# Kernel optimization log

Measured on AMD Instinct MI355X. Metric: run time of the kernel, lower is better.

The kernel has to match this reference:

```python
import jax, jax.numpy as jnp
import numpy as np

HIDDEN = 1024
HEADS = 16
HEAD_DIM = HIDDEN // HEADS


def setup_inputs() -> dict:
    key = jax.random.key(0)
    ks = jax.random.split(key, 9)
    B, S = 2, 2048
    std = 0.02
    inp = {
        "query": jax.random.normal(ks[0], (B, S, HIDDEN), dtype=jnp.float32),
        "Wq": jax.random.normal(ks[1], (HIDDEN, HIDDEN), dtype=jnp.float32) * std,
        "bq": jnp.zeros((HIDDEN,), dtype=jnp.float32),
        "Wk": jax.random.normal(ks[2], (HIDDEN, HIDDEN), dtype=jnp.float32) * std,
        "bk": jnp.zeros((HIDDEN,), dtype=jnp.float32),
        "Wv": jax.random.normal(ks[3], (HIDDEN, HIDDEN), dtype=jnp.float32) * std,
        "bv": jnp.zeros((HIDDEN,), dtype=jnp.float32),
        "Wo": jax.random.normal(ks[4], (HIDDEN, HIDDEN), dtype=jnp.float32) * std,
        "bo": jnp.zeros((HIDDEN,), dtype=jnp.float32),
    }
    return inp


def reference(query, Wq, bq, Wk, bk, Wv, bv, Wo, bo):
    B, S, H = query.shape
    # torch nn.Linear: y = x @ W.T + b
    Q = query @ Wq.T + bq
    K = query @ Wk.T + bk  # key defaults to query (self-attention)
    V = query @ Wv.T + bv
    # [B, S, H] -> [B, heads, S, head_dim]
    def split_heads(x):
        return x.reshape(B, S, HEADS, HEAD_DIM).transpose(0, 2, 1, 3)
    Qh, Kh, Vh = split_heads(Q), split_heads(K), split_heads(V)
    scale = jnp.sqrt(jnp.asarray(HEAD_DIM, dtype=query.dtype))
    scores = jnp.einsum("bhqd,bhkd->bhqk", Qh, Kh) / scale
    attn = jax.nn.softmax(scores, axis=-1)  # dropout=0 (eval)
    context = jnp.einsum("bhqk,bhkd->bhqd", attn, Vh)
    context = context.transpose(0, 2, 1, 3).reshape(B, S, H)
    output = context @ Wo.T + bo
    return output, attn
```

## Files before the change

### kernel.cpp

```cpp
#include <hip/hip_runtime.h>
#include <hip/hip_bf16.h>
#include <cstdint>

typedef __attribute__((ext_vector_type(4))) float f32x4;
typedef __attribute__((ext_vector_type(8))) short bf16x8;

__device__ __forceinline__ unsigned short f2bf(float f){
  union { float f; unsigned int u; } v; v.f = f;
  unsigned int u = v.u;
  u += 0x7FFFu + ((u >> 16) & 1u);
  return (unsigned short)(u >> 16);
}
__device__ __forceinline__ float bf2f(unsigned short s){
  union { unsigned int u; float f; } v; v.u = ((unsigned int)s) << 16;
  return v.f;
}

__global__ __launch_bounds__(256) void cvt_bf16(const float* __restrict__ in,
                                                unsigned short* __restrict__ out,
                                                int n4){
  int i = blockIdx.x * 256 + threadIdx.x;
  if (i < n4){
    float4 v = ((const float4*)in)[i];
    ushort4 o;
    o.x = f2bf(v.x); o.y = f2bf(v.y); o.z = f2bf(v.z); o.w = f2bf(v.w);
    ((ushort4*)out)[i] = o;
  }
}

__global__ __launch_bounds__(256) void qkv_gemm(
    const unsigned short* __restrict__ A,
    const unsigned short* __restrict__ W0,
    const unsigned short* __restrict__ W1,
    const unsigned short* __restrict__ W2,
    const float* __restrict__ b0,
    const float* __restrict__ b1,
    const float* __restrict__ b2,
    unsigned short* __restrict__ Qo,
    unsigned short* __restrict__ Khead,
    unsigned short* __restrict__ Vto)
{
  __shared__ unsigned short As[2][128*64];
  __shared__ unsigned short Bs[2][128*64];

  const int K = 1024;
  const int tid = threadIdx.x;
  const int l   = tid & 63;
  const int wid = tid >> 6;
  const int g   = l >> 4;
  const int li  = l & 15;
  const int widx = blockIdx.x >> 3;
  const int m0  = blockIdx.y * 128;
  const int n0  = (blockIdx.x & 7) * 128;
  const int wm  = (wid >> 1) * 64;
  const int wn  = (wid & 1) * 64;
  const int srow = tid >> 3;
  const int sck  = tid & 7;

  const unsigned short* Bw = (widx == 0) ? W0 : ((widx == 1) ? W1 : W2);
  const float* bias        = (widx == 0) ? b0 : ((widx == 1) ? b1 : b2);

  const unsigned short* Ag = A  + (size_t)(m0 + srow) * K + sck * 8;
  const unsigned short* Bg = Bw + (size_t)(n0 + srow) * K + sck * 8;

  f32x4 acc[4][4] = {};
  bf16x8 ra[4], rb[4];
  const int NT = K >> 6;

  #pragma unroll
  for (int r = 0; r < 4; ++r){
    ra[r] = *(const bf16x8*)(Ag + (size_t)(r*32) * K);
    rb[r] = *(const bf16x8*)(Bg + (size_t)(r*32) * K);
  }
  #pragma unroll
  for (int r = 0; r < 4; ++r){
    const int row = srow + r*32;
    const int ck  = sck ^ (row & 7);
    *(bf16x8*)(&As[0][row*64 + ck*8]) = ra[r];
    *(bf16x8*)(&Bs[0][row*64 + ck*8]) = rb[r];
  }
  __syncthreads();

  int cur = 0;
  for (int kt = 0; kt < NT; ++kt){
    if (kt + 1 < NT){
      const int kof = (kt + 1) << 6;
      #pragma unroll
      for (int r = 0; r < 4; ++r){
        ra[r] = *(const bf16x8*)(Ag + (size_t)(r*32) * K + kof);
        rb[r] = *(const bf16x8*)(Bg + (size_t)(r*32) * K + kof);
      }
    }
    #pragma unroll
    for (int kk = 0; kk < 2; ++kk){
      bf16x8 af[4], bfr[4];
      #pragma unroll
      for (int f = 0; f < 4; ++f){
        const int rowa = wm + f*16 + li;
        const int cka  = (kk*4 + g) ^ (rowa & 7);
        af[f] = *(const bf16x8*)(&As[cur][rowa*64 + cka*8]);
        const int rowb = wn + f*16 + li;
        const int ckb  = (kk*4 + g) ^ (rowb & 7);
        bfr[f] = *(const bf16x8*)(&Bs[cur][rowb*64 + ckb*8]);
      }
      #pragma unroll
      for (int fm = 0; fm < 4; ++fm)
        #pragma unroll
        for (int fn = 0; fn < 4; ++fn)
          acc[fm][fn] = __builtin_amdgcn_mfma_f32_16x16x32_bf16(af[fm], bfr[fn], acc[fm][fn], 0, 0, 0);
    }
    __syncthreads();
    if (kt + 1 < NT){
      #pragma unroll
      for (int r = 0; r < 4; ++r){
        const int row = srow + r*32;
        const int ck  = sck ^ (row & 7);
        *(bf16x8*)(&As[cur^1][row*64 + ck*8]) = ra[r];
        *(bf16x8*)(&Bs[cur^1][row*64 + ck*8]) = rb[r];
      }
      __syncthreads();
    }
    cur ^= 1;
  }

  #pragma unroll
  for (int fn = 0; fn < 4; ++fn){
    const int col = n0 + wn + fn*16 + li;
    const float bv = bias[col];
    #pragma unroll
    for (int fm = 0; fm < 4; ++fm){
      #pragma unroll
      for (int j = 0; j < 4; ++j){
        const int row = m0 + wm + fm*16 + g*4 + j;
        const float v = acc[fm][fn][j] + bv;
        const int bb = row >> 11;
        const int s  = row & 2047;
        if (widx == 0){
          Qo[(size_t)row * 1024 + col] = f2bf(v);
        } else if (widx == 1){
          const int hh = col >> 6, dd = col & 63;
          Khead[(((size_t)(bb*16 + hh))*2048 + s)*64 + dd] = f2bf(v);
        } else {
          Vto[((size_t)(bb*1024 + col)) * 2048 + s] = f2bf(v);
        }
      }
    }
  }
}

__global__ __launch_bounds__(256) void gemm_bt(
    const unsigned short* __restrict__ A,
    const unsigned short* __restrict__ Bw,
    const float* __restrict__ bias,
    float* __restrict__ outp,
    int M, int N, int K)
{
  __shared__ unsigned short As[2][128*64];
  __shared__ unsigned short Bs[2][128*64];

  const int tid = threadIdx.x;
  const int l   = tid & 63;
  const int wid = tid >> 6;
  const int g   = l >> 4;
  const int li  = l & 15;
  const int m0  = blockIdx.y * 128;
  const int n0  = blockIdx.x * 128;
  const int wm  = (wid >> 1) * 64;
  const int wn  = (wid & 1) * 64;
  const int srow = tid >> 3;
  const int sck  = tid & 7;

  const unsigned short* Ag = A  + (size_t)(m0 + srow) * K + sck * 8;
  const unsigned short* Bg = Bw + (size_t)(n0 + srow) * K + sck * 8;

  f32x4 acc[4][4] = {};
  bf16x8 ra[4], rb[4];
  const int NT = K >> 6;

  #pragma unroll
  for (int r = 0; r < 4; ++r){
    ra[r] = *(const bf16x8*)(Ag + (size_t)(r*32) * K);
    rb[r] = *(const bf16x8*)(Bg + (size_t)(r*32) * K);
  }
  #pragma unroll
  for (int r = 0; r < 4; ++r){
    const int row = srow + r*32;
    const int ck  = sck ^ (row & 7);
    *(bf16x8*)(&As[0][row*64 + ck*8]) = ra[r];
    *(bf16x8*)(&Bs[0][row*64 + ck*8]) = rb[r];
  }
  __syncthreads();

  int cur = 0;
  for (int kt = 0; kt < NT; ++kt){
    if (kt + 1 < NT){
      const int kof = (kt + 1) << 6;
      #pragma unroll
      for (int r = 0; r < 4; ++r){
        ra[r] = *(const bf16x8*)(Ag + (size_t)(r*32) * K + kof);
        rb[r] = *(const bf16x8*)(Bg + (size_t)(r*32) * K + kof);
      }
    }
    #pragma unroll
    for (int kk = 0; kk < 2; ++kk){
      bf16x8 af[4], bfr[4];
      #pragma unroll
      for (int f = 0; f < 4; ++f){
        const int rowa = wm + f*16 + li;
        const int cka  = (kk*4 + g) ^ (rowa & 7);
        af[f] = *(const bf16x8*)(&As[cur][rowa*64 + cka*8]);
        const int rowb = wn + f*16 + li;
        const int ckb  = (kk*4 + g) ^ (rowb & 7);
        bfr[f] = *(const bf16x8*)(&Bs[cur][rowb*64 + ckb*8]);
      }
      #pragma unroll
      for (int fm = 0; fm < 4; ++fm)
        #pragma unroll
        for (int fn = 0; fn < 4; ++fn)
          acc[fm][fn] = __builtin_amdgcn_mfma_f32_16x16x32_bf16(af[fm], bfr[fn], acc[fm][fn], 0, 0, 0);
    }
    __syncthreads();
    if (kt + 1 < NT){
      #pragma unroll
      for (int r = 0; r < 4; ++r){
        const int row = srow + r*32;
        const int ck  = sck ^ (row & 7);
        *(bf16x8*)(&As[cur^1][row*64 + ck*8]) = ra[r];
        *(bf16x8*)(&Bs[cur^1][row*64 + ck*8]) = rb[r];
      }
      __syncthreads();
    }
    cur ^= 1;
  }

  #pragma unroll
  for (int fn = 0; fn < 4; ++fn){
    const int col = n0 + wn + fn*16 + li;
    const float bv = bias[col];
    #pragma unroll
    for (int fm = 0; fm < 4; ++fm){
      #pragma unroll
      for (int j = 0; j < 4; ++j){
        const int row = m0 + wm + fm*16 + g*4 + j;
        outp[(size_t)row * N + col] = acc[fm][fn][j] + bv;
      }
    }
  }
}

__global__ __launch_bounds__(256, 4) void attn_denom(
    const unsigned short* __restrict__ Qb,
    const unsigned short* __restrict__ Khead,
    float* __restrict__ denomP)
{
  __shared__ unsigned short Ks[256*64];
  char* Kb8 = (char*)Ks;

  const int tid = threadIdx.x;
  const int l   = tid & 63;
  const int w   = tid >> 6;
  const int g   = l >> 4;
  const int li  = l & 15;
  const int kt  = blockIdx.x >> 5;
  const int bh  = blockIdx.x & 31;
  const int qt  = blockIdx.y;
  const int b   = bh >> 4;
  const int h   = bh & 15;

  {
    const unsigned short* Kg = Khead + ((size_t)bh * 2048 + kt*256) * 64;
    #pragma unroll
    for (int p = 0; p < 8; ++p){
      const int key = p*32 + (tid >> 3);
      const int c   = tid & 7;
      const bf16x8 v = *(const bf16x8*)(Kg + (size_t)key * 64 + c*8);
      *(bf16x8*)(Kb8 + key*128 + ((c ^ (key & 7)) * 16)) = v;
    }
  }
  __syncthreads();

  #pragma unroll
  for (int rg = 0; rg < 2; ++rg){
    const int qrow = qt*128 + w*32 + rg*16 + li;
    const size_t qoff = (size_t)(b*2048 + qrow) * 1024 + h*64 + g*8;
    const bf16x8 aq0 = *(const bf16x8*)(Qb + qoff);
    const bf16x8 aq1 = *(const bf16x8*)(Qb + qoff + 32);

    float ls = 0.f;
    #pragma unroll
    for (int cf = 0; cf < 16; ++cf){
      const int key = cf*16 + li;
      const bf16x8 k0 = *(const bf16x8*)(Kb8 + key*128 + (( g    ^ (key & 7)) * 16));
      const bf16x8 k1 = *(const bf16x8*)(Kb8 + key*128 + (((g+4) ^ (key & 7)) * 16));
      f32x4 t = {};
      t = __builtin_amdgcn_mfma_f32_16x16x32_bf16(k0, aq0, t, 0, 0, 0);
      t = __builtin_amdgcn_mfma_f32_16x16x32_bf16(k1, aq1, t, 0, 0, 0);
      ls += __expf(t[0]*0.125f) + __expf(t[1]*0.125f)
          + __expf(t[2]*0.125f) + __expf(t[3]*0.125f);
    }
    ls += __shfl_xor(ls, 16);
    ls += __shfl_xor(ls, 32);
    if (l < 16)
      denomP[((size_t)kt*32 + bh)*2048 + qt*128 + w*32 + rg*16 + l] = ls;
  }
}

__global__ __launch_bounds__(256, 2) void attn_pass(
    const unsigned short* __restrict__ Qb,
    const unsigned short* __restrict__ Khead,
    const unsigned short* __restrict__ Vt,
    const float* __restrict__ denomP,
    float* __restrict__ attn,
    float* __restrict__ CP)
{
  __shared__ unsigned short Ks[256*64];
  __shared__ __align__(16) unsigned short Pw4[4][16*256];
  char* Kb8 = (char*)Ks;

  const int tid = threadIdx.x;
  const int l   = tid & 63;
  const int w   = tid >> 6;
  const int g   = l >> 4;
  const int li  = l & 15;
  const int kt  = blockIdx.x >> 5;
  const int bh  = blockIdx.x & 31;
  const int qt  = blockIdx.y;
  const int b   = bh >> 4;
  const int h   = bh & 15;

  {
    const unsigned short* Kg = Khead + ((size_t)bh * 2048 + kt*256) * 64;
    #pragma unroll
    for (int p = 0; p < 8; ++p){
      const int key = p*32 + (tid >> 3);
      const int c   = tid & 7;
      const bf16x8 v = *(const bf16x8*)(Kg + (size_t)key * 64 + c*8);
      *(bf16x8*)(Kb8 + key*128 + ((c ^ (key & 7)) * 16)) = v;
    }
  }
  __syncthreads();

  char* myP = (char*)(&Pw4[w][0]);
  const int swz = (li & 7) << 3;
  const unsigned short* Vbase = Vt + (size_t)(b*1024 + h*64) * 2048 + kt*256;

  f32x4 acc0[4] = {};
  f32x4 acc1[4] = {};

  #pragma unroll
  for (int rg = 0; rg < 2; ++rg){
    const int qbase = qt*128 + w*32 + rg*16;
    const int qrow  = qbase + li;

    float ds = 0.f;
    #pragma unroll
    for (int k2 = 0; k2 < 8; ++k2)
      ds += denomP[((size_t)k2*32 + bh)*2048 + qrow];
    const float rv = 1.0f / ds;

    const size_t qoff = (size_t)(b*2048 + qrow) * 1024 + h*64 + g*8;
    const bf16x8 aq0 = *(const bf16x8*)(Qb + qoff);
    const bf16x8 aq1 = *(const bf16x8*)(Qb + qoff + 32);

    #pragma unroll
    for (int cf = 0; cf < 16; ++cf){
      const int key = cf*16 + li;
      const bf16x8 k0 = *(const bf16x8*)(Kb8 + key*128 + (( g    ^ (key & 7)) * 16));
      const bf16x8 k1 = *(const bf16x8*)(Kb8 + key*128 + (((g+4) ^ (key & 7)) * 16));
      f32x4 t = {};
      t = __builtin_amdgcn_mfma_f32_16x16x32_bf16(k0, aq0, t, 0, 0, 0);
      t = __builtin_amdgcn_mfma_f32_16x16x32_bf16(k1, aq1, t, 0, 0, 0);
      ushort4 u;
      u.x = f2bf(__expf(t[0]*0.125f) * rv);
      u.y = f2bf(__expf(t[1]*0.125f) * rv);
      u.z = f2bf(__expf(t[2]*0.125f) * rv);
      u.w = f2bf(__expf(t[3]*0.125f) * rv);
      const int colb = cf*32 + g*8;
      *(ushort4*)(myP + li*512 + (colb ^ swz)) = u;
    }

    #pragma unroll
    for (int r = 0; r < 16; ++r){
      const ushort4 u = *(const ushort4*)(myP + r*512 + ((l*8) ^ ((r & 7) << 3)));
      f32x4 o;
      o[0] = bf2f(u.x); o[1] = bf2f(u.y); o[2] = bf2f(u.z); o[3] = bf2f(u.w);
      *(f32x4*)(attn + ((size_t)bh*2048 + qbase + r)*2048 + kt*256 + l*4) = o;
    }

    #pragma unroll
    for (int ks = 0; ks < 8; ++ks){
      const int colb2 = ks*64 + g*16;
      const ushort4 plo = *(const ushort4*)(myP + li*512 + ( colb2      ^ swz));
      const ushort4 phi = *(const ushort4*)(myP + li*512 + ((colb2 + 8) ^ swz));
      bf16x8 pa;
      pa[0] = plo.x; pa[1] = plo.y; pa[2] = plo.z; pa[3] = plo.w;
      pa[4] = phi.x; pa[5] = phi.y; pa[6] = phi.z; pa[7] = phi.w;
      #pragma unroll
      for (int df = 0; df < 4; ++df){
        const bf16x8 vb = *(const bf16x8*)(Vbase + (size_t)(df*16 + li) * 2048 + ks*32 + g*8);
        if (rg == 0) acc0[df] = __builtin_amdgcn_mfma_f32_16x16x32_bf16(vb, pa, acc0[df], 0, 0, 0);
        else         acc1[df] = __builtin_amdgcn_mfma_f32_16x16x32_bf16(vb, pa, acc1[df], 0, 0, 0);
      }
    }
  }

  #pragma unroll
  for (int rg = 0; rg < 2; ++rg){
    const int qrow = qt*128 + w*32 + rg*16 + li;
    #pragma unroll
    for (int df = 0; df < 4; ++df){
      const f32x4 v = (rg == 0) ? acc0[df] : acc1[df];
      *(f32x4*)(CP + (((size_t)kt*32 + bh)*2048 + qrow)*64 + df*16 + g*4) = v;
    }
  }
}

__global__ __launch_bounds__(256) void ctx_reduce(
    const float* __restrict__ CP,
    unsigned short* __restrict__ Cb)
{
  const int idx = blockIdx.x * 256 + threadIdx.x;
  const int bh  = idx >> 15;
  const int rem = idx & 32767;
  const int q   = rem >> 4;
  const int d4  = (rem & 15) << 2;
  f32x4 s = {};
  #pragma unroll
  for (int kt = 0; kt < 8; ++kt){
    const f32x4 v = *(const f32x4*)(CP + (((size_t)kt*32 + bh)*2048 + q)*64 + d4);
    s[0] += v[0]; s[1] += v[1]; s[2] += v[2]; s[3] += v[3];
  }
  const int b = bh >> 4, h = bh & 15;
  ushort4 o;
  o.x = f2bf(s[0]); o.y = f2bf(s[1]); o.z = f2bf(s[2]); o.w = f2bf(s[3]);
  *(ushort4*)(Cb + (size_t)(b*2048 + q)*1024 + h*64 + d4) = o;
}

extern "C" void kernel_launch(void* const* d_in, const int* in_sizes, int n_in,
                              void* d_out, int out_size, void* d_ws, size_t ws_size,
                              hipStream_t stream)
{
  const float* X  = (const float*)d_in[0];
  const float* Wq = (const float*)d_in[1];
  const float* bq = (const float*)d_in[2];
  const float* Wk = (const float*)d_in[3];
  const float* bk = (const float*)d_in[4];
  const float* Wv = (const float*)d_in[5];
  const float* bv = (const float*)d_in[6];
  const float* Wo = (const float*)d_in[7];
  const float* bo = (const float*)d_in[8];

  char* ws = (char*)d_ws;
  unsigned short* Xb    = (unsigned short*)(ws);
  unsigned short* Qb    = (unsigned short*)(ws + (size_t)( 8u<<20));
  unsigned short* Khead = (unsigned short*)(ws + (size_t)(16u<<20));
  unsigned short* Vt    = (unsigned short*)(ws + (size_t)(24u<<20));
  unsigned short* Cb    = (unsigned short*)(ws + (size_t)(32u<<20));
  unsigned short* Wqb   = (unsigned short*)(ws + (size_t)(40u<<20));
  unsigned short* Wkb   = (unsigned short*)(ws + (size_t)(42u<<20));
  unsigned short* Wvb   = (unsigned short*)(ws + (size_t)(44u<<20));
  unsigned short* Wob   = (unsigned short*)(ws + (size_t)(46u<<20));
  float*          denomP= (float*)(ws + (size_t)(48u<<20));
  float*          CP    = (float*)(ws + (size_t)(56u<<20));

  float* out  = (float*)d_out;
  float* attn = out + (size_t)4194304;

  cvt_bf16<<<4096, 256, 0, stream>>>(X,  Xb,  1048576);
  cvt_bf16<<<1024, 256, 0, stream>>>(Wq, Wqb, 262144);
  cvt_bf16<<<1024, 256, 0, stream>>>(Wk, Wkb, 262144);
  cvt_bf16<<<1024, 256, 0, stream>>>(Wv, Wvb, 262144);
  cvt_bf16<<<1024, 256, 0, stream>>>(Wo, Wob, 262144);

  dim3 qkvgrid(24, 32);
  qkv_gemm<<<qkvgrid, 256, 0, stream>>>(Xb, Wqb, Wkb, Wvb, bq, bk, bv, Qb, Khead, Vt);

  dim3 agrid(256, 16);
  attn_denom<<<agrid, 256, 0, stream>>>(Qb, Khead, denomP);
  attn_pass<<<agrid, 256, 0, stream>>>(Qb, Khead, Vt, denomP, attn, CP);

  ctx_reduce<<<4096, 256, 0, stream>>>(CP, Cb);

  dim3 ggrid(8, 32);
  gemm_bt<<<ggrid, 256, 0, stream>>>(Cb, Wob, bo, out, 4096, 1024, 1024);
}
```

Measured before the change: 363.5 us.

## Fuse attention denominator, probability pass and context reduction into one kernel

Replaces the separate denominator kernel, the split-key attention pass and the context reduction kernel with a single kernel. Each block owns 64 query rows of one head and loops over all eight key tiles twice: once for the softmax denominator, once to write probabilities and accumulate P·V in registers. This removes the partial-denominator and partial-context buffers, their global round trips and two launches. In exchange there are fewer blocks (1024 vs 4096), serialized key-tile loops with barriers, and the K tiles are reloaded for the second pass. It also pads the K rows in shared memory, batches the V loads, and uses nontemporal stores for the attention output.

```diff
diff --git a/kernel.cpp b/kernel.cpp
--- a/kernel.cpp
+++ b/kernel.cpp
@@ -248,125 +248,87 @@
   }
 }
 
-__global__ __launch_bounds__(256, 4) void attn_denom(
+__global__ __launch_bounds__(256, 2) void attn_all(
     const unsigned short* __restrict__ Qb,
     const unsigned short* __restrict__ Khead,
-    float* __restrict__ denomP)
+    const unsigned short* __restrict__ Vt,
+    float* __restrict__ attn,
+    unsigned short* __restrict__ ctxb)
 {
-  __shared__ unsigned short Ks[256*64];
-  char* Kb8 = (char*)Ks;
+  __shared__ __align__(16) char Kb8[256*144];
+  __shared__ __align__(16) unsigned short Pw4[4][16*256];
 
   const int tid = threadIdx.x;
   const int l   = tid & 63;
   const int w   = tid >> 6;
   const int g   = l >> 4;
   const int li  = l & 15;
-  const int kt  = blockIdx.x >> 5;
   const int bh  = blockIdx.x & 31;
-  const int qt  = blockIdx.y;
+  const int qt  = blockIdx.x >> 5;
   const int b   = bh >> 4;
   const int h   = bh & 15;
 
-  {
-    const unsigned short* Kg = Khead + ((size_t)bh * 2048 + kt*256) * 64;
-    #pragma unroll
-    for (int p = 0; p < 8; ++p){
-      const int key = p*32 + (tid >> 3);
-      const int c   = tid & 7;
-      const bf16x8 v = *(const bf16x8*)(Kg + (size_t)key * 64 + c*8);
-      *(bf16x8*)(Kb8 + key*128 + ((c ^ (key & 7)) * 16)) = v;
-    }
-  }
-  __syncthreads();
-
-  #pragma unroll
-  for (int rg = 0; rg < 2; ++rg){
-    const int qrow = qt*128 + w*32 + rg*16 + li;
-    const size_t qoff = (size_t)(b*2048 + qrow) * 1024 + h*64 + g*8;
-    const bf16x8 aq0 = *(const bf16x8*)(Qb + qoff);
-    const bf16x8 aq1 = *(const bf16x8*)(Qb + qoff + 32);
-
-    float ls = 0.f;
+  const int qrow = qt*64 + w*16 + li;
+  const size_t qoff = (size_t)(b*2048 + qrow) * 1024 + h*64 + g*8;
+  const bf16x8 aq0 = *(const bf16x8*)(Qb + qoff);
+  const bf16x8 aq1 = *(const bf16x8*)(Qb + qoff + 32);
+  const unsigned short* Kg0 = Khead + (size_t)bh * (2048*64);
+
+  float ls = 0.f;
+  for (int kt = 0; kt < 8; ++kt){
+    __syncthreads();
+    {
+      const unsigned short* Kg = Kg0 + (size_t)kt * (256*64);
+      #pragma unroll
+      for (int p = 0; p < 8; ++p){
+        const int key = p*32 + (tid >> 3);
+        const int c   = tid & 7;
+        const bf16x8 v = *(const bf16x8*)(Kg + (size_t)key*64 + c*8);
+        *(bf16x8*)(Kb8 + key*144 + ((c ^ (key & 7)) * 16)) = v;
+      }
+    }
+    __syncthreads();
     #pragma unroll
     for (int cf = 0; cf < 16; ++cf){
       const int key = cf*16 + li;
-      const bf16x8 k0 = *(const bf16x8*)(Kb8 + key*128 + (( g    ^ (key & 7)) * 16));
-      const bf16x8 k1 = *(const bf16x8*)(Kb8 + key*128 + (((g+4) ^ (key & 7)) * 16));
+      const bf16x8 k0 = *(const bf16x8*)(Kb8 + key*144 + (( g    ^ (key & 7)) * 16));
+      const bf16x8 k1 = *(const bf16x8*)(Kb8 + key*144 + (((g+4) ^ (key & 7)) * 16));
       f32x4 t = {};
       t = __builtin_amdgcn_mfma_f32_16x16x32_bf16(k0, aq0, t, 0, 0, 0);
       t = __builtin_amdgcn_mfma_f32_16x16x32_bf16(k1, aq1, t, 0, 0, 0);
       ls += __expf(t[0]*0.125f) + __expf(t[1]*0.125f)
           + __expf(t[2]*0.125f) + __expf(t[3]*0.125f);
     }
-    ls += __shfl_xor(ls, 16);
-    ls += __shfl_xor(ls, 32);
-    if (l < 16)
-      denomP[((size_t)kt*32 + bh)*2048 + qt*128 + w*32 + rg*16 + l] = ls;
-  }
-}
-
-__global__ __launch_bounds__(256, 2) void attn_pass(
-    const unsigned short* __restrict__ Qb,
-    const unsigned short* __restrict__ Khead,
-    const unsigned short* __restrict__ Vt,
-    const float* __restrict__ denomP,
-    float* __restrict__ attn,
-    float* __restrict__ CP)
-{
-  __shared__ unsigned short Ks[256*64];
-  __shared__ __align__(16) unsigned short Pw4[4][16*256];
-  char* Kb8 = (char*)Ks;
-
-  const int tid = threadIdx.x;
-  const int l   = tid & 63;
-  const int w   = tid >> 6;
-  const int g   = l >> 4;
-  const int li  = l & 15;
-  const int kt  = blockIdx.x >> 5;
-  const int bh  = blockIdx.x & 31;
-  const int qt  = blockIdx.y;
-  const int b   = bh >> 4;
-  const int h   = bh & 15;
-
-  {
-    const unsigned short* Kg = Khead + ((size_t)bh * 2048 + kt*256) * 64;
-    #pragma unroll
-    for (int p = 0; p < 8; ++p){
-      const int key = p*32 + (tid >> 3);
-      const int c   = tid & 7;
-      const bf16x8 v = *(const bf16x8*)(Kg + (size_t)key * 64 + c*8);
-      *(bf16x8*)(Kb8 + key*128 + ((c ^ (key & 7)) * 16)) = v;
-    }
-  }
-  __syncthreads();
-
+  }
+  ls += __shfl_xor(ls, 16);
+  ls += __shfl_xor(ls, 32);
+  const float rv = 1.0f / ls;
+
+  f32x4 pv[4] = {};
   char* myP = (char*)(&Pw4[w][0]);
   const int swz = (li & 7) << 3;
-  const unsigned short* Vbase = Vt + (size_t)(b*1024 + h*64) * 2048 + kt*256;
-
-  f32x4 acc0[4] = {};
-  f32x4 acc1[4] = {};
-
-  #pragma unroll
-  for (int rg = 0; rg < 2; ++rg){
-    const int qbase = qt*128 + w*32 + rg*16;
-    const int qrow  = qbase + li;
-
-    float ds = 0.f;
-    #pragma unroll
-    for (int k2 = 0; k2 < 8; ++k2)
-      ds += denomP[((size_t)k2*32 + bh)*2048 + qrow];
-    const float rv = 1.0f / ds;
-
-    const size_t qoff = (size_t)(b*2048 + qrow) * 1024 + h*64 + g*8;
-    const bf16x8 aq0 = *(const bf16x8*)(Qb + qoff);
-    const bf16x8 aq1 = *(const bf16x8*)(Qb + qoff + 32);
+  const unsigned short* Vb0 = Vt + (size_t)(b*1024 + h*64) * 2048;
+  float* arow0 = attn + ((size_t)bh*2048 + qt*64 + w*16) * 2048;
+
+  for (int kt = 0; kt < 8; ++kt){
+    __syncthreads();
+    {
+      const unsigned short* Kg = Kg0 + (size_t)kt * (256*64);
+      #pragma unroll
+      for (int p = 0; p < 8; ++p){
+        const int key = p*32 + (tid >> 3);
+        const int c   = tid & 7;
+        const bf16x8 v = *(const bf16x8*)(Kg + (size_t)key*64 + c*8);
+        *(bf16x8*)(Kb8 + key*144 + ((c ^ (key & 7)) * 16)) = v;
+      }
+    }
+    __syncthreads();
 
     #pragma unroll
     for (int cf = 0; cf < 16; ++cf){
       const int key = cf*16 + li;
-      const bf16x8 k0 = *(const bf16x8*)(Kb8 + key*128 + (( g    ^ (key & 7)) * 16));
-      const bf16x8 k1 = *(const bf16x8*)(Kb8 + key*128 + (((g+4) ^ (key & 7)) * 16));
+      const bf16x8 k0 = *(const bf16x8*)(Kb8 + key*144 + (( g    ^ (key & 7)) * 16));
+      const bf16x8 k1 = *(const bf16x8*)(Kb8 + key*144 + (((g+4) ^ (key & 7)) * 16));
       f32x4 t = {};
       t = __builtin_amdgcn_mfma_f32_16x16x32_bf16(k0, aq0, t, 0, 0, 0);
       t = __builtin_amdgcn_mfma_f32_16x16x32_bf16(k1, aq1, t, 0, 0, 0);
@@ -375,8 +337,30 @@
       u.y = f2bf(__expf(t[1]*0.125f) * rv);
       u.z = f2bf(__expf(t[2]*0.125f) * rv);
       u.w = f2bf(__expf(t[3]*0.125f) * rv);
-      const int colb = cf*32 + g*8;
-      *(ushort4*)(myP + li*512 + (colb ^ swz)) = u;
+      *(ushort4*)(myP + li*512 + ((cf*32 + g*8) ^ swz)) = u;
+    }
+
+    #pragma unroll
+    for (int vh = 0; vh < 2; ++vh){
+      bf16x8 vb[16];
+      #pragma unroll
+      for (int ks = 0; ks < 4; ++ks)
+        #pragma unroll
+        for (int df = 0; df < 4; ++df)
+          vb[ks*4+df] = *(const bf16x8*)(Vb0 + (size_t)(df*16 + li)*2048
+                                         + kt*256 + (vh*4+ks)*32 + g*8);
+      #pragma unroll
+      for (int ks = 0; ks < 4; ++ks){
+        const int colb = (vh*4+ks)*64 + g*16;
+        const ushort4 plo = *(const ushort4*)(myP + li*512 + ( colb      ^ swz));
+        const ushort4 phi = *(const ushort4*)(myP + li*512 + ((colb + 8) ^ swz));
+        bf16x8 pa;
+        pa[0] = plo.x; pa[1] = plo.y; pa[2] = plo.z; pa[3] = plo.w;
+        pa[4] = phi.x; pa[5] = phi.y; pa[6] = phi.z; pa[7] = phi.w;
+        #pragma unroll
+        for (int df = 0; df < 4; ++df)
+          pv[df] = __builtin_amdgcn_mfma_f32_16x16x32_bf16(pa, vb[ks*4+df], pv[df], 0, 0, 0);
+      }
     }
 
     #pragma unroll
@@ -384,56 +368,16 @@
       const ushort4 u = *(const ushort4*)(myP + r*512 + ((l*8) ^ ((r & 7) << 3)));
       f32x4 o;
       o[0] = bf2f(u.x); o[1] = bf2f(u.y); o[2] = bf2f(u.z); o[3] = bf2f(u.w);
-      *(f32x4*)(attn + ((size_t)bh*2048 + qbase + r)*2048 + kt*256 + l*4) = o;
-    }
-
-    #pragma unroll
-    for (int ks = 0; ks < 8; ++ks){
-      const int colb2 = ks*64 + g*16;
-      const ushort4 plo = *(const ushort4*)(myP + li*512 + ( colb2      ^ swz));
-      const ushort4 phi = *(const ushort4*)(myP + li*512 + ((colb2 + 8) ^ swz));
-      bf16x8 pa;
-      pa[0] = plo.x; pa[1] = plo.y; pa[2] = plo.z; pa[3] = plo.w;
-      pa[4] = phi.x; pa[5] = phi.y; pa[6] = phi.z; pa[7] = phi.w;
-      #pragma unroll
-      for (int df = 0; df < 4; ++df){
-        const bf16x8 vb = *(const bf16x8*)(Vbase + (size_t)(df*16 + li) * 2048 + ks*32 + g*8);
-        if (rg == 0) acc0[df] = __builtin_amdgcn_mfma_f32_16x16x32_bf16(vb, pa, acc0[df], 0, 0, 0);
-        else         acc1[df] = __builtin_amdgcn_mfma_f32_16x16x32_bf16(vb, pa, acc1[df], 0, 0, 0);
-      }
-    }
-  }
-
-  #pragma unroll
-  for (int rg = 0; rg < 2; ++rg){
-    const int qrow = qt*128 + w*32 + rg*16 + li;
-    #pragma unroll
-    for (int df = 0; df < 4; ++df){
-      const f32x4 v = (rg == 0) ? acc0[df] : acc1[df];
-      *(f32x4*)(CP + (((size_t)kt*32 + bh)*2048 + qrow)*64 + df*16 + g*4) = v;
-    }
-  }
-}
-
-__global__ __launch_bounds__(256) void ctx_reduce(
-    const float* __restrict__ CP,
-    unsigned short* __restrict__ Cb)
-{
-  const int idx = blockIdx.x * 256 + threadIdx.x;
-  const int bh  = idx >> 15;
-  const int rem = idx & 32767;
-  const int q   = rem >> 4;
-  const int d4  = (rem & 15) << 2;
-  f32x4 s = {};
-  #pragma unroll
-  for (int kt = 0; kt < 8; ++kt){
-    const f32x4 v = *(const f32x4*)(CP + (((size_t)kt*32 + bh)*2048 + q)*64 + d4);
-    s[0] += v[0]; s[1] += v[1]; s[2] += v[2]; s[3] += v[3];
-  }
-  const int b = bh >> 4, h = bh & 15;
-  ushort4 o;
-  o.x = f2bf(s[0]); o.y = f2bf(s[1]); o.z = f2bf(s[2]); o.w = f2bf(s[3]);
-  *(ushort4*)(Cb + (size_t)(b*2048 + q)*1024 + h*64 + d4) = o;
+      __builtin_nontemporal_store(o, (f32x4*)(arow0 + (size_t)r*2048 + kt*256 + l*4));
+    }
+  }
+
+  #pragma unroll
+  for (int df = 0; df < 4; ++df)
+    #pragma unroll
+    for (int j = 0; j < 4; ++j)
+      ctxb[(size_t)(b*2048 + qt*64 + w*16 + g*4 + j)*1024 + h*64 + df*16 + li]
+        = f2bf(pv[df][j]);
 }
 
 extern "C" void kernel_launch(void* const* d_in, const int* in_sizes, int n_in,
@@ -460,8 +404,6 @@
   unsigned short* Wkb   = (unsigned short*)(ws + (size_t)(42u<<20));
   unsigned short* Wvb   = (unsigned short*)(ws + (size_t)(44u<<20));
   unsigned short* Wob   = (unsigned short*)(ws + (size_t)(46u<<20));
-  float*          denomP= (float*)(ws + (size_t)(48u<<20));
-  float*          CP    = (float*)(ws + (size_t)(56u<<20));
 
   float* out  = (float*)d_out;
   float* attn = out + (size_t)4194304;
@@ -475,11 +417,7 @@
   dim3 qkvgrid(24, 32);
   qkv_gemm<<<qkvgrid, 256, 0, stream>>>(Xb, Wqb, Wkb, Wvb, bq, bk, bv, Qb, Khead, Vt);
 
-  dim3 agrid(256, 16);
-  attn_denom<<<agrid, 256, 0, stream>>>(Qb, Khead, denomP);
-  attn_pass<<<agrid, 256, 0, stream>>>(Qb, Khead, Vt, denomP, attn, CP);
-
-  ctx_reduce<<<4096, 256, 0, stream>>>(CP, Cb);
+  attn_all<<<dim3(1024), 256, 0, stream>>>(Qb, Khead, Vt, attn, Cb);
 
   dim3 ggrid(8, 32);
   gemm_bt<<<ggrid, 256, 0, stream>>>(Cb, Wob, bo, out, 4096, 1024, 1024);
```

Result: faster. 338.8 us, median of 2 (-6.8%).

## Restructure attention pass to drop LDS K staging and halve key splits

Applied to the files above, without the earlier changes.

Reworks the attention pass so each block handles 64 query rows over 512 keys. K and V fragments are loaded directly from global memory into registers in batches instead of staging K in shared memory behind a barrier. Occupancy is raised to four blocks per CU, the attn output uses nontemporal stores, and there are half as many context partials to reduce. The four weight conversions are also merged into one launch. The cost is more redundant global reads of K and higher register pressure from the batched fragments.

```diff
diff --git a/kernel.cpp b/kernel.cpp
--- a/kernel.cpp
+++ b/kernel.cpp
@@ -26,6 +26,24 @@
     o.x = f2bf(v.x); o.y = f2bf(v.y); o.z = f2bf(v.z); o.w = f2bf(v.w);
     ((ushort4*)out)[i] = o;
   }
+}
+
+__global__ __launch_bounds__(256) void cvt_w4(const float* __restrict__ W0,
+                                              const float* __restrict__ W1,
+                                              const float* __restrict__ W2,
+                                              const float* __restrict__ W3,
+                                              unsigned short* __restrict__ o0,
+                                              unsigned short* __restrict__ o1,
+                                              unsigned short* __restrict__ o2,
+                                              unsigned short* __restrict__ o3){
+  const int wi = blockIdx.y;
+  const float* in = (wi == 0) ? W0 : (wi == 1) ? W1 : (wi == 2) ? W2 : W3;
+  unsigned short* out = (wi == 0) ? o0 : (wi == 1) ? o1 : (wi == 2) ? o2 : o3;
+  int i = blockIdx.x * 256 + threadIdx.x;
+  float4 v = ((const float4*)in)[i];
+  ushort4 o;
+  o.x = f2bf(v.x); o.y = f2bf(v.y); o.z = f2bf(v.z); o.w = f2bf(v.w);
+  ((ushort4*)out)[i] = o;
 }
 
 __global__ __launch_bounds__(256) void qkv_gemm(
@@ -305,7 +323,7 @@
   }
 }
 
-__global__ __launch_bounds__(256, 2) void attn_pass(
+__global__ __launch_bounds__(256, 4) void attn_pass4(
     const unsigned short* __restrict__ Qb,
     const unsigned short* __restrict__ Khead,
     const unsigned short* __restrict__ Vt,
@@ -313,70 +331,86 @@
     float* __restrict__ attn,
     float* __restrict__ CP)
 {
-  __shared__ unsigned short Ks[256*64];
   __shared__ __align__(16) unsigned short Pw4[4][16*256];
-  char* Kb8 = (char*)Ks;
 
   const int tid = threadIdx.x;
   const int l   = tid & 63;
   const int w   = tid >> 6;
   const int g   = l >> 4;
   const int li  = l & 15;
-  const int kt  = blockIdx.x >> 5;
+  const int kt2 = blockIdx.x >> 5;
   const int bh  = blockIdx.x & 31;
   const int qt  = blockIdx.y;
   const int b   = bh >> 4;
   const int h   = bh & 15;
 
-  {
-    const unsigned short* Kg = Khead + ((size_t)bh * 2048 + kt*256) * 64;
-    #pragma unroll
-    for (int p = 0; p < 8; ++p){
-      const int key = p*32 + (tid >> 3);
-      const int c   = tid & 7;
-      const bf16x8 v = *(const bf16x8*)(Kg + (size_t)key * 64 + c*8);
-      *(bf16x8*)(Kb8 + key*128 + ((c ^ (key & 7)) * 16)) = v;
-    }
-  }
-  __syncthreads();
-
+  const int qrow = qt*64 + w*16 + li;
+  const size_t qoff = (size_t)(b*2048 + qrow) * 1024 + h*64 + g*8;
+  const bf16x8 aq0 = *(const bf16x8*)(Qb + qoff);
+  const bf16x8 aq1 = *(const bf16x8*)(Qb + qoff + 32);
+  const unsigned short* Kg0 = Khead + (size_t)bh * (2048*64) + g*8;
+
+  float dsum = 0.f;
+  #pragma unroll
+  for (int k2 = 0; k2 < 8; ++k2)
+    dsum += denomP[((size_t)k2*32 + bh)*2048 + qrow];
+  const float rv = 1.0f / dsum;
+
+  f32x4 pv[4] = {};
   char* myP = (char*)(&Pw4[w][0]);
   const int swz = (li & 7) << 3;
-  const unsigned short* Vbase = Vt + (size_t)(b*1024 + h*64) * 2048 + kt*256;
-
-  f32x4 acc0[4] = {};
-  f32x4 acc1[4] = {};
-
-  #pragma unroll
-  for (int rg = 0; rg < 2; ++rg){
-    const int qbase = qt*128 + w*32 + rg*16;
-    const int qrow  = qbase + li;
-
-    float ds = 0.f;
-    #pragma unroll
-    for (int k2 = 0; k2 < 8; ++k2)
-      ds += denomP[((size_t)k2*32 + bh)*2048 + qrow];
-    const float rv = 1.0f / ds;
-
-    const size_t qoff = (size_t)(b*2048 + qrow) * 1024 + h*64 + g*8;
-    const bf16x8 aq0 = *(const bf16x8*)(Qb + qoff);
-    const bf16x8 aq1 = *(const bf16x8*)(Qb + qoff + 32);
-
-    #pragma unroll
-    for (int cf = 0; cf < 16; ++cf){
-      const int key = cf*16 + li;
-      const bf16x8 k0 = *(const bf16x8*)(Kb8 + key*128 + (( g    ^ (key & 7)) * 16));
-      const bf16x8 k1 = *(const bf16x8*)(Kb8 + key*128 + (((g+4) ^ (key & 7)) * 16));
-      f32x4 t = {};
-      t = __builtin_amdgcn_mfma_f32_16x16x32_bf16(k0, aq0, t, 0, 0, 0);
-      t = __builtin_amdgcn_mfma_f32_16x16x32_bf16(k1, aq1, t, 0, 0, 0);
-      ushort4 u;
-      u.x = f2bf(__expf(t[0]*0.125f) * rv);
-      u.y = f2bf(__expf(t[1]*0.125f) * rv);
-      u.z = f2bf(__expf(t[2]*0.125f) * rv);
-      u.w = f2bf(__expf(t[3]*0.125f) * rv);
-      const int colb = cf*32 + g*8;
-      *(ushort4*)(myP + li*512 + (colb ^ swz)) = u;
+  const unsigned short* Vb0 = Vt + (size_t)(b*1024 + h*64) * 2048;
+  float* arow0 = attn + ((size_t)bh*2048 + qt*64 + w*16) * 2048;
+
+  #pragma unroll
+  for (int t = 0; t < 2; ++t){
+    const int kbase = kt2*512 + t*256;
+
+    #pragma unroll
+    for (int half = 0; half < 2; ++half){
+      bf16x8 bk[16];
+      #pragma unroll
+      for (int cf = 0; cf < 8; ++cf){
+        const unsigned short* kr = Kg0 + (size_t)(kbase + half*128 + cf*16 + li) * 64;
+        bk[cf*2]   = *(const bf16x8*)(kr);
+        bk[cf*2+1] = *(const bf16x8*)(kr + 32);
+      }
+      #pragma unroll
+      for (int cf = 0; cf < 8; ++cf){
+        f32x4 s = {};
+        s = __builtin_amdgcn_mfma_f32_16x16x32_bf16(bk[cf*2],   aq0, s, 0, 0, 0);
+        s = __builtin_amdgcn_mfma_f32_16x16x32_bf16(bk[cf*2+1], aq1, s, 0, 0, 0);
+        ushort4 u;
+        u.x = f2bf(__expf(s[0]*0.125f) * rv);
+        u.y = f2bf(__expf(s[1]*0.125f) * rv);
+        u.z = f2bf(__expf(s[2]*0.125f) * rv);
+        u.w = f2bf(__expf(s[3]*0.125f) * rv);
+        const int colb = half*256 + cf*32 + g*8;
+        *(ushort4*)(myP + li*512 + (colb ^ swz)) = u;
+      }
+    }
+
+    #pragma unroll
+    for (int vh = 0; vh < 2; ++vh){
+      bf16x8 vb[16];
+      #pragma unroll
+      for (int ks = 0; ks < 4; ++ks)
+        #pragma unroll
+        for (int df = 0; df < 4; ++df)
+          vb[ks*4+df] = *(const bf16x8*)(Vb0 + (size_t)(df*16 + li)*2048
+                                         + kbase + (vh*4+ks)*32 + g*8);
+      #pragma unroll
+      for (int ks = 0; ks < 4; ++ks){
+        const int colb = (vh*4+ks)*64 + g*16;
+        const ushort4 plo = *(const ushort4*)(myP + li*512 + ( colb      ^ swz));
+        const ushort4 phi = *(const ushort4*)(myP + li*512 + ((colb + 8) ^ swz));
+        bf16x8 pa;
+        pa[0] = plo.x; pa[1] = plo.y; pa[2] = plo.z; pa[3] = plo.w;
+        pa[4] = phi.x; pa[5] = phi.y; pa[6] = phi.z; pa[7] = phi.w;
+        #pragma unroll
+        for (int df = 0; df < 4; ++df)
+          pv[df] = __builtin_amdgcn_mfma_f32_16x16x32_bf16(pa, vb[ks*4+df], pv[df], 0, 0, 0);
+      }
     }
 
     #pragma unroll
@@ -384,38 +418,19 @@
       const ushort4 u = *(const ushort4*)(myP + r*512 + ((l*8) ^ ((r & 7) << 3)));
       f32x4 o;
       o[0] = bf2f(u.x); o[1] = bf2f(u.y); o[2] = bf2f(u.z); o[3] = bf2f(u.w);
-      *(f32x4*)(attn + ((size_t)bh*2048 + qbase + r)*2048 + kt*256 + l*4) = o;
-    }
-
-    #pragma unroll
-    for (int ks = 0; ks < 8; ++ks){
-      const int colb2 = ks*64 + g*16;
-      const ushort4 plo = *(const ushort4*)(myP + li*512 + ( colb2      ^ swz));
-      const ushort4 phi = *(const ushort4*)(myP + li*512 + ((colb2 + 8) ^ swz));
-      bf16x8 pa;
-      pa[0] = plo.x; pa[1] = plo.y; pa[2] = plo.z; pa[3] = plo.w;
-      pa[4] = phi.x; pa[5] = phi.y; pa[6] = phi.z; pa[7] = phi.w;
-      #pragma unroll
-      for (int df = 0; df < 4; ++df){
-        const bf16x8 vb = *(const bf16x8*)(Vbase + (size_t)(df*16 + li) * 2048 + ks*32 + g*8);
-        if (rg == 0) acc0[df] = __builtin_amdgcn_mfma_f32_16x16x32_bf16(vb, pa, acc0[df], 0, 0, 0);
-        else         acc1[df] = __builtin_amdgcn_mfma_f32_16x16x32_bf16(vb, pa, acc1[df], 0, 0, 0);
-      }
-    }
-  }
-
-  #pragma unroll
-  for (int rg = 0; rg < 2; ++rg){
-    const int qrow = qt*128 + w*32 + rg*16 + li;
-    #pragma unroll
-    for (int df = 0; df < 4; ++df){
-      const f32x4 v = (rg == 0) ? acc0[df] : acc1[df];
-      *(f32x4*)(CP + (((size_t)kt*32 + bh)*2048 + qrow)*64 + df*16 + g*4) = v;
-    }
-  }
-}
-
-__global__ __launch_bounds__(256) void ctx_reduce(
+      __builtin_nontemporal_store(o, (f32x4*)(arow0 + (size_t)r*2048 + kbase + l*4));
+    }
+  }
+
+  #pragma unroll
+  for (int df = 0; df < 4; ++df)
+    #pragma unroll
+    for (int j = 0; j < 4; ++j)
+      CP[(((size_t)kt2*32 + bh)*2048 + qt*64 + w*16 + g*4 + j)*64 + df*16 + li]
+        = pv[df][j];
+}
+
+__global__ __launch_bounds__(256) void ctx_reduce4(
     const float* __restrict__ CP,
     unsigned short* __restrict__ Cb)
 {
@@ -426,8 +441,8 @@
   const int d4  = (rem & 15) << 2;
   f32x4 s = {};
   #pragma unroll
-  for (int kt = 0; kt < 8; ++kt){
-    const f32x4 v = *(const f32x4*)(CP + (((size_t)kt*32 + bh)*2048 + q)*64 + d4);
+  for (int k2 = 0; k2 < 4; ++k2){
+    const f32x4 v = *(const f32x4*)(CP + (((size_t)k2*32 + bh)*2048 + q)*64 + d4);
     s[0] += v[0]; s[1] += v[1]; s[2] += v[2]; s[3] += v[3];
   }
   const int b = bh >> 4, h = bh & 15;
@@ -466,20 +481,15 @@
   float* out  = (float*)d_out;
   float* attn = out + (size_t)4194304;
 
-  cvt_bf16<<<4096, 256, 0, stream>>>(X,  Xb,  1048576);
-  cvt_bf16<<<1024, 256, 0, stream>>>(Wq, Wqb, 262144);
-  cvt_bf16<<<1024, 256, 0, stream>>>(Wk, Wkb, 262144);
-  cvt_bf16<<<1024, 256, 0, stream>>>(Wv, Wvb, 262144);
-  cvt_bf16<<<1024, 256, 0, stream>>>(Wo, Wob, 262144);
+  cvt_bf16<<<4096, 256, 0, stream>>>(X, Xb, 1048576);
+  cvt_w4<<<dim3(1024, 4), 256, 0, stream>>>(Wq, Wk, Wv, Wo, Wqb, Wkb, Wvb, Wob);
 
   dim3 qkvgrid(24, 32);
   qkv_gemm<<<qkvgrid, 256, 0, stream>>>(Xb, Wqb, Wkb, Wvb, bq, bk, bv, Qb, Khead, Vt);
 
-  dim3 agrid(256, 16);
-  attn_denom<<<agrid, 256, 0, stream>>>(Qb, Khead, denomP);
-  attn_pass<<<agrid, 256, 0, stream>>>(Qb, Khead, Vt, denomP, attn, CP);
-
-  ctx_reduce<<<4096, 256, 0, stream>>>(CP, Cb);
+  attn_denom<<<dim3(256, 16), 256, 0, stream>>>(Qb, Khead, denomP);
+  attn_pass4<<<dim3(128, 32), 256, 0, stream>>>(Qb, Khead, Vt, denomP, attn, CP);
+  ctx_reduce4<<<4096, 256, 0, stream>>>(CP, Cb);
 
   dim3 ggrid(8, 32);
   gemm_bt<<<ggrid, 256, 0, stream>>>(Cb, Wob, bo, out, 4096, 1024, 1024);
```

After: 408.4 us. +12.3%, slower.
